# Kernel tuning notes

Hardware: AMD Instinct MI355X
Metric: run time of the kernel (lower is better)

The kernel has to match this reference:

```python
import jax, jax.numpy as jnp
import numpy as np

B, D = 1024, 768


def setup_inputs() -> dict:
    key = jax.random.key(0)
    k1, k2 = jax.random.split(key)
    image_features = jax.random.normal(k1, (B, D), dtype=jnp.float32)
    # plant a few exact duplicate rows so the label-propagation path is nontrivial
    image_features = image_features.at[17].set(image_features[3])
    image_features = image_features.at[512].set(image_features[3])
    image_features = image_features.at[900].set(image_features[128])
    text_features = jax.random.normal(k2, (B, D), dtype=jnp.float32)
    logit_scale = jnp.float32(14.285714)  # exp(log(1/0.07)), standard CLIP init
    return {"image_features": image_features, "text_features": text_features, "logit_scale": logit_scale}


def reference(image_features, text_features, logit_scale):
    # logits_per_image: [B, B]
    logits = logit_scale * (image_features @ text_features.T)
    # Duplicate detection: the original O(B^2) python loop assigns to row j the
    # index of the FIRST row i (i <= j) whose features exactly equal row j.
    # eq[i, j] = rows i and j are elementwise identical
    eq = jnp.all(image_features[:, None, :] == image_features[None, :, :], axis=-1)  # [B, B] bool
    labels = jnp.argmax(eq, axis=0)  # first matching index per row (diag guarantees a hit)
    # cross-entropy with integer labels, mean over batch
    logp = jax.nn.log_softmax(logits, axis=1)
    loss = -jnp.mean(jnp.take_along_axis(logp, labels[:, None], axis=1))
    return loss
```

## Files before the change

kernel.cpp:

```cpp
#include <hip/hip_runtime.h>
#include <stdint.h>

#define BATCH 1024
#define DIM 768

typedef unsigned long long u64;
typedef __attribute__((ext_vector_type(8))) short short8;
typedef __attribute__((ext_vector_type(4))) float f32x4;

#define WS_TAIL     0
#define WS_PMAX  4096
#define WS_PSUM 20480
#define WS_LVAL 36864

__device__ __forceinline__ unsigned short to_bf16(float x) {
    unsigned int u = __float_as_uint(x);
    return (unsigned short)((u + 0x7FFFu + ((u >> 16) & 1u)) >> 16);
}

__device__ __forceinline__ short8 cvt8(const float4 a, const float4 b) {
    short8 r = {(short)to_bf16(a.x), (short)to_bf16(a.y),
                (short)to_bf16(a.z), (short)to_bf16(a.w),
                (short)to_bf16(b.x), (short)to_bf16(b.y),
                (short)to_bf16(b.z), (short)to_bf16(b.w)};
    return r;
}

__global__ __launch_bounds__(1024) void fused_kernel(
        const float* __restrict__ img, const float* __restrict__ txt,
        const float* __restrict__ scale_p,
        float* __restrict__ pmax, float* __restrict__ psum,
        float* __restrict__ lval, int* __restrict__ tailcnt,
        float* __restrict__ out) {
    __shared__ __align__(16) char smem[24 * 1024 + 2 * 16 * 1024];
    unsigned short* Ahi = (unsigned short*)smem;
    unsigned short* Bb[2] = {(unsigned short*)(smem + 24 * 1024),
                             (unsigned short*)(smem + 40 * 1024)};
    float* logitsS = (float*)(smem + 24 * 1024);
    __shared__ int isLast;
    __shared__ float part[16];

    const int tid  = threadIdx.x;
    const int wave = tid >> 6;
    const int lane = tid & 63;
    const int quad = lane >> 4;
    const int l15  = lane & 15;
    const int r0    = (blockIdx.x >> 2) * 16;
    const int chunk = blockIdx.x & 3;

    const int c   = tid >> 2;
    const int sub = tid & 3;
    const float* sp = txt + (size_t)(chunk * 256 + c) * DIM + sub * 8;
    const int woff = (c >> 4) * 512 + sub * 128 + (c & 15) * 8;

    {
        const float* ir = img + (size_t)(r0 + wave) * DIM;
#pragma unroll
        for (int j = 0; j < 12; ++j) {
            const int k = lane + j * 64;
            Ahi[((k >> 3) * 16 + wave) * 8 + (k & 7)] = to_bf16(ir[k]);
        }
    }

    {
        const float4 va = *(const float4*)(sp);
        const float4 vb = *(const float4*)(sp + 4);
        *(short8*)(Bb[0] + woff) = cvt8(va, vb);
    }
    __syncthreads();

    const int foff = quad * 128 + l15 * 8;
    f32x4 acc = {0.f, 0.f, 0.f, 0.f};
#pragma unroll
    for (int kk = 0; kk < 24; ++kk) {
        float4 na, nb;
        if (kk < 23) {
            na = *(const float4*)(sp + (kk + 1) * 32);
            nb = *(const float4*)(sp + (kk + 1) * 32 + 4);
        }
        const short8 a = *(const short8*)&Ahi[kk * 512 + foff];
        const short8 b = *(const short8*)&Bb[kk & 1][wave * 512 + foff];
        acc = __builtin_amdgcn_mfma_f32_16x16x32_bf16(a, b, acc, 0, 0, 0);
        if (kk < 23)
            *(short8*)(Bb[(kk + 1) & 1] + woff) = cvt8(na, nb);
        __syncthreads();
    }

    const float scale = scale_p[0];
#pragma unroll
    for (int r = 0; r < 4; ++r)
        logitsS[(quad * 4 + r) * 260 + wave * 16 + l15] = scale * acc[r];
    __syncthreads();

    {
        const float4 f = *(const float4*)&logitsS[wave * 260 + lane * 4];
        float mx = fmaxf(fmaxf(f.x, f.y), fmaxf(f.z, f.w));
#pragma unroll
        for (int s = 32; s; s >>= 1) mx = fmaxf(mx, __shfl_xor(mx, s, 64));
        float sum = __expf(f.x - mx) + __expf(f.y - mx) +
                    __expf(f.z - mx) + __expf(f.w - mx);
#pragma unroll
        for (int s = 32; s; s >>= 1) sum += __shfl_xor(sum, s, 64);
        if (lane == 0) {
            atomicExch(&pmax[(r0 + wave) * 4 + chunk], mx);
            atomicExch(&psum[(r0 + wave) * 4 + chunk], sum);
        }
    }

    if (wave < 4) {
        const int j = r0 + chunk * 4 + wave;
        const float2 sj = *(const float2*)(img + (size_t)j * DIM);
        int lo = -1;
        int label = j;
        for (;;) {
            int cand = BATCH;
#pragma unroll
            for (int it = 0; it < 16; ++it) {
                const int i = lane + it * 64;
                const float2 si = *(const float2*)(img + (size_t)i * DIM);
                if (i < j && i > lo && si.x == sj.x && si.y == sj.y)
                    cand = min(cand, i);
            }
#pragma unroll
            for (int s = 32; s; s >>= 1) cand = min(cand, __shfl_xor(cand, s, 64));
            if (cand >= j) break;
            const float4* rpm = (const float4*)(img + (size_t)cand * DIM);
            const float4* rpj = (const float4*)(img + (size_t)j * DIM);
            bool eq = true;
#pragma unroll
            for (int cc = 0; cc < 3; ++cc) {
                float4 vm = rpm[cc * 64 + lane];
                float4 vj = rpj[cc * 64 + lane];
                eq = eq && (vm.x == vj.x) && (vm.y == vj.y) &&
                     (vm.z == vj.z) && (vm.w == vj.w);
            }
            if (__all(eq)) { label = cand; break; }
            lo = cand;
        }

        const float4* aj = (const float4*)(img + (size_t)j * DIM);
        const float4* bl = (const float4*)(txt + (size_t)label * DIM);
        float s = 0.0f;
#pragma unroll
        for (int cc = 0; cc < 3; ++cc) {
            const float4 va = aj[cc * 64 + lane];
            const float4 vb = bl[cc * 64 + lane];
            s += va.x * vb.x + va.y * vb.y + va.z * vb.z + va.w * vb.w;
        }
#pragma unroll
        for (int m = 32; m; m >>= 1) s += __shfl_xor(s, m, 64);
        if (lane == 0) atomicExch(&lval[j], scale * s);
    }

    __syncthreads();
    if (tid == 0) {
        __threadfence();
        isLast = (atomicAdd(tailcnt, 1) == (int)gridDim.x - 1) ? 1 : 0;
    }
    __syncthreads();
    if (!isLast) return;
    __threadfence();

    {
        const float4 m4 = *(const float4*)&pmax[tid * 4];
        const float4 s4 = *(const float4*)&psum[tid * 4];
        const float lv = lval[tid];
        const float gmax = fmaxf(fmaxf(m4.x, m4.y), fmaxf(m4.z, m4.w));
        const float ss = s4.x * __expf(m4.x - gmax) + s4.y * __expf(m4.y - gmax)
                       + s4.z * __expf(m4.z - gmax) + s4.w * __expf(m4.w - gmax);
        float loss = gmax + __logf(ss) - lv;
#pragma unroll
        for (int m = 32; m; m >>= 1) loss += __shfl_xor(loss, m, 64);
        if (lane == 0) part[wave] = loss;
        __syncthreads();
        if (tid == 0) {
            float tot = 0.0f;
#pragma unroll
            for (int w = 0; w < 16; ++w) tot += part[w];
            out[0] = tot * (1.0f / BATCH);
        }
    }
}

extern "C" void kernel_launch(void* const* d_in, const int* in_sizes, int n_in,
                              void* d_out, int out_size, void* d_ws, size_t ws_size,
                              hipStream_t stream) {
    const float* img   = (const float*)d_in[0];
    const float* txt   = (const float*)d_in[1];
    const float* scale = (const float*)d_in[2];
    float* out = (float*)d_out;
    char* ws = (char*)d_ws;

    int*   tailcnt = (int*)(ws + WS_TAIL);
    float* pmax    = (float*)(ws + WS_PMAX);
    float* psum    = (float*)(ws + WS_PSUM);
    float* lval    = (float*)(ws + WS_LVAL);

    hipMemsetAsync(ws + WS_TAIL, 0, 4, stream);
    fused_kernel<<<256, 1024, 0, stream>>>(img, txt, scale,
                                           pmax, psum, lval, tailcnt, out);
}
```

Measured before the change: 95.38 us.

## Load text operands straight to registers and drop per-step LDS staging and barriers

Each wave now loads its own 16 text rows directly from global memory into a six-deep register ring and converts them to bf16 right before the MFMA. This removes the shared-memory double buffer for B and the __syncthreads in all 24 K-steps. The release fence before the tail-counter atomic is also removed. The cost is more registers per thread and less coalesced global loads (16 rows per wave rather than a shared cooperative tile). Dropping the fence risks the last block reading stale partial results, since the writes use atomicExch but no fence orders them before the counter increment.

```diff
diff --git a/kernel.cpp b/kernel.cpp
--- a/kernel.cpp
+++ b/kernel.cpp
@@ -32,11 +32,8 @@
         float* __restrict__ pmax, float* __restrict__ psum,
         float* __restrict__ lval, int* __restrict__ tailcnt,
         float* __restrict__ out) {
-    __shared__ __align__(16) char smem[24 * 1024 + 2 * 16 * 1024];
-    unsigned short* Ahi = (unsigned short*)smem;
-    unsigned short* Bb[2] = {(unsigned short*)(smem + 24 * 1024),
-                             (unsigned short*)(smem + 40 * 1024)};
-    float* logitsS = (float*)(smem + 24 * 1024);
+    __shared__ unsigned short Ahi[16 * DIM];
+    __shared__ float logitsS[16 * 260];
     __shared__ int isLast;
     __shared__ float part[16];
 
@@ -48,10 +45,15 @@
     const int r0    = (blockIdx.x >> 2) * 16;
     const int chunk = blockIdx.x & 3;
 
-    const int c   = tid >> 2;
-    const int sub = tid & 3;
-    const float* sp = txt + (size_t)(chunk * 256 + c) * DIM + sub * 8;
-    const int woff = (c >> 4) * 512 + sub * 128 + (c & 15) * 8;
+    const int t = chunk * 16 + wave;
+    const float* tp = txt + (size_t)(t * 16 + l15) * DIM + quad * 8;
+
+    float4 ra[6], rb[6];
+#pragma unroll
+    for (int i = 0; i < 6; ++i) {
+        ra[i] = *(const float4*)(tp + i * 32);
+        rb[i] = *(const float4*)(tp + i * 32 + 4);
+    }
 
     {
         const float* ir = img + (size_t)(r0 + wave) * DIM;
@@ -61,29 +63,19 @@
             Ahi[((k >> 3) * 16 + wave) * 8 + (k & 7)] = to_bf16(ir[k]);
         }
     }
-
-    {
-        const float4 va = *(const float4*)(sp);
-        const float4 vb = *(const float4*)(sp + 4);
-        *(short8*)(Bb[0] + woff) = cvt8(va, vb);
-    }
     __syncthreads();
 
     const int foff = quad * 128 + l15 * 8;
     f32x4 acc = {0.f, 0.f, 0.f, 0.f};
 #pragma unroll
     for (int kk = 0; kk < 24; ++kk) {
-        float4 na, nb;
-        if (kk < 23) {
-            na = *(const float4*)(sp + (kk + 1) * 32);
-            nb = *(const float4*)(sp + (kk + 1) * 32 + 4);
+        const short8 a = *(const short8*)&Ahi[kk * 512 + foff];
+        const short8 b = cvt8(ra[kk % 6], rb[kk % 6]);
+        acc = __builtin_amdgcn_mfma_f32_16x16x32_bf16(a, b, acc, 0, 0, 0);
+        if (kk + 6 < 24) {
+            ra[kk % 6] = *(const float4*)(tp + (kk + 6) * 32);
+            rb[kk % 6] = *(const float4*)(tp + (kk + 6) * 32 + 4);
         }
-        const short8 a = *(const short8*)&Ahi[kk * 512 + foff];
-        const short8 b = *(const short8*)&Bb[kk & 1][wave * 512 + foff];
-        acc = __builtin_amdgcn_mfma_f32_16x16x32_bf16(a, b, acc, 0, 0, 0);
-        if (kk < 23)
-            *(short8*)(Bb[(kk + 1) & 1] + woff) = cvt8(na, nb);
-        __syncthreads();
     }
 
     const float scale = scale_p[0];
@@ -153,10 +145,8 @@
     }
 
     __syncthreads();
-    if (tid == 0) {
-        __threadfence();
+    if (tid == 0)
         isLast = (atomicAdd(tailcnt, 1) == (int)gridDim.x - 1) ? 1 : 0;
-    }
     __syncthreads();
     if (!isLast) return;
     __threadfence();
```

New measurement: 95.97 us. No clear change (+0.6%).
